# Kernel tuning notes

Measured on AMD Instinct MI355X. Metric: run time of the kernel, lower is better.

## Reference

```python
import jax, jax.numpy as jnp
import numpy as np

B, N = 1, 512
NODE_DIM, EDGE_DIM = 384, 128
H, SK, SV, PK, PV = 8, 16, 16, 4, 4
EPS = 1e-8
LN_EPS = 1e-5


def setup_inputs() -> dict:
    key = jax.random.key(0)
    ks = jax.random.split(key, 20)
    d, e = NODE_DIM, EDGE_DIM
    s = 0.02
    rn = lambda k, sh: jax.random.normal(k, sh, jnp.float32) * s
    # orthonormal per-residue rotations (valid rigid frames)
    R, _ = jnp.linalg.qr(jax.random.normal(ks[2], (B, N, 3, 3), jnp.float32))
    out_dim = H * (SV + EDGE_DIM + PV * 4)  # scalar + pairwise + points(3) + point norms(1)
    return dict(
        node_features=jax.random.normal(ks[0], (B, N, d), jnp.float32),
        edge_features=jax.random.normal(ks[1], (B, N, N, e), jnp.float32),
        rotations=R,
        translations=jax.random.normal(ks[3], (B, N, 3), jnp.float32),
        mask=jnp.ones((B, N), bool),
        Wq_s=rn(ks[4], (d, H * SK)), Wk_s=rn(ks[5], (d, H * SK)), Wv_s=rn(ks[6], (d, H * SV)),
        Wq_p=rn(ks[7], (d, H * PK * 3)), Wk_p=rn(ks[8], (d, H * PK * 3)), Wv_p=rn(ks[9], (d, H * PV * 3)),
        point_weights=jnp.full((H,), np.log(np.e - 1.0), jnp.float32),  # softplus -> 1
        Wb=rn(ks[10], (e, H)), bb=jnp.zeros((H,), jnp.float32),
        Wo=rn(ks[11], (out_dim, d)), bo=jnp.zeros((d,), jnp.float32),
        g1=jnp.ones((d,), jnp.float32), beta1=jnp.zeros((d,), jnp.float32),
        W1=rn(ks[12], (d, 2 * d)), b1=jnp.zeros((2 * d,), jnp.float32),
        W2=rn(ks[13], (2 * d, 2 * d)), b2=jnp.zeros((2 * d,), jnp.float32),
        W3=rn(ks[14], (2 * d, d)), b3=jnp.zeros((d,), jnp.float32),
        g2=jnp.ones((d,), jnp.float32), beta2=jnp.zeros((d,), jnp.float32),
    )


def _layer_norm(x, g, b):
    mu = x.mean(-1, keepdims=True)
    var = ((x - mu) ** 2).mean(-1, keepdims=True)
    return (x - mu) * jax.lax.rsqrt(var + LN_EPS) * g + b


def _forward(node_features, edge_features, rotations, translations, mask,
             Wq_s, Wk_s, Wv_s, Wq_p, Wk_p, Wv_p, point_weights, Wb, bb, Wo, bo,
             g1, beta1, W1, b1, W2, b2, W3, b3, g2, beta2):
    b, n, d = node_features.shape
    # num_attn_logits = 3 (scalar + point + pairwise)
    scal_scale = (3 * SK) ** -0.5
    point_scale = (3 * PK * 4.5) ** -0.5
    pair_scale = 3 ** -0.5

    qs = (node_features @ Wq_s).reshape(b, n, H, SK)
    kk = (node_features @ Wk_s).reshape(b, n, H, SK)
    vs = (node_features @ Wv_s).reshape(b, n, H, SV)

    def apply_rigid(p):  # p: (b,n,h,d,3); global = R^T applied per lucidrains einsum + t
        return jnp.einsum('bnhdc,bncr->bnhdr', p, rotations) + translations[:, :, None, None, :]

    qp = apply_rigid((node_features @ Wq_p).reshape(b, n, H, PK, 3))
    kp = apply_rigid((node_features @ Wk_p).reshape(b, n, H, PK, 3))
    vp = apply_rigid((node_features @ Wv_p).reshape(b, n, H, PV, 3))

    logits = jnp.einsum('bihk,bjhk->bhij', qs, kk) * scal_scale

    # point distance term: sum_{d,c} (q-k)^2 = |q|^2 + |k|^2 - 2 q.k (avoids (b,h,i,j,d,3) tensor)
    w = jax.nn.softplus(point_weights)  # (H,)
    q2 = jnp.einsum('bnhdc,bnhdc->bhn', qp, qp)
    k2 = jnp.einsum('bnhdc,bnhdc->bhn', kp, kp)
    cross = jnp.einsum('bihdc,bjhdc->bhij', qp, kp)
    dist = q2[..., :, None] + k2[..., None, :] - 2.0 * cross  # (b,h,i,j)
    logits = logits - 0.5 * point_scale * w[None, :, None, None] * dist

    pair_bias = (jnp.einsum('bije,eh->bhij', edge_features, Wb) + bb[None, :, None, None]) * pair_scale
    logits = logits + pair_bias

    pm = mask[:, None, :, None] & mask[:, None, None, :]  # (b,1,i,j)
    logits = jnp.where(pm, logits, -jnp.finfo(logits.dtype).max)
    attn = jax.nn.softmax(logits, axis=-1)  # (b,h,i,j)

    rs = jnp.einsum('bhij,bjhv->bihv', attn, vs).reshape(b, n, H * SV)
    rp = jnp.einsum('bhij,bije->bihe', attn, edge_features).reshape(b, n, H * EDGE_DIM)
    pts = jnp.einsum('bhij,bjhdc->bihdc', attn, vp)
    # invert rigid: subtract t, apply R (inverse of R^T application)
    local = jnp.einsum('bihdc,birc->bihdr', pts - translations[:, :, None, None, :], rotations)
    norms = jnp.sqrt((local ** 2).sum(-1) + EPS)  # (b,n,H,PV)

    cat = jnp.concatenate([rs, local.reshape(b, n, H * PV * 3), norms.reshape(b, n, H * PV), rp], axis=-1)
    ipa_out = cat @ Wo + bo

    x = _layer_norm(ipa_out, g1, beta1)  # dropout is identity at eval
    x = jax.nn.relu(x @ W1 + b1)
    x = jax.nn.relu(x @ W2 + b2)
    x = x @ W3 + b3
    return _layer_norm(x, g2, beta2)


def reference(node_features, edge_features, rotations, translations, mask,
              Wq_s, Wk_s, Wv_s, Wq_p, Wk_p, Wv_p, point_weights, Wb, bb, Wo, bo,
              g1, beta1, W1, b1, W2, b2, W3, b3, g2, beta2):
    return _forward(node_features, edge_features, rotations, translations, mask,
                    Wq_s, Wk_s, Wv_s, Wq_p, Wk_p, Wv_p, point_weights, Wb, bb, Wo, bo,
                    g1, beta1, W1, b1, W2, b2, W3, b3, g2, beta2)
```

## Files before the change

kernel.cpp:

```cpp
#include <hip/hip_runtime.h>
#include <cstddef>

#define NN 512
#define DD 384
#define EE 128
#define HH 8

static constexpr float SCAL_SCALE  = 0.1443375673f;
static constexpr float POINT_SCALE = 0.1360827635f;
static constexpr float PAIR_SCALE  = 0.5773502692f;
static constexpr float LN_EPS = 1e-5f;
static constexpr float EPS    = 1e-8f;

typedef __bf16 bf16x8 __attribute__((ext_vector_type(8)));
typedef float  f32x4  __attribute__((ext_vector_type(4)));

__device__ __forceinline__ unsigned short bf16_bits(float v) {
    union { __bf16 b; unsigned short s; } c; c.b = (__bf16)v; return c.s;
}

__global__ __launch_bounds__(256) void prep_weights_kernel(
    const float* __restrict__ Wo, const float* __restrict__ W1,
    const float* __restrict__ W2, const float* __restrict__ W3,
    const float* __restrict__ Wq_s, const float* __restrict__ Wk_s,
    const float* __restrict__ Wv_s,
    const float* __restrict__ Wq_p, const float* __restrict__ Wk_p,
    const float* __restrict__ Wv_p,
    unsigned short* __restrict__ WoT, unsigned short* __restrict__ W1T,
    unsigned short* __restrict__ W2T, unsigned short* __restrict__ W3T,
    unsigned short* __restrict__ WprojT)
{
    const int b = blockIdx.x;
    const float* W; unsigned short* out;
    int K, N, tile, rowoff = 0;
    if (b < 480)       { W = Wo;   out = WoT;    K = 1280; N = 384; tile = b; }
    else if (b < 768)  { W = W1;   out = W1T;    K = 384;  N = 768; tile = b - 480; }
    else if (b < 1344) { W = W2;   out = W2T;    K = 768;  N = 768; tile = b - 768; }
    else if (b < 1632) { W = W3;   out = W3T;    K = 768;  N = 384; tile = b - 1344; }
    else if (b < 1680) { W = Wq_s; out = WprojT; K = 384;  N = 128; tile = b - 1632; rowoff = 0; }
    else if (b < 1728) { W = Wk_s; out = WprojT; K = 384;  N = 128; tile = b - 1680; rowoff = 128; }
    else if (b < 1776) { W = Wv_s; out = WprojT; K = 384;  N = 128; tile = b - 1728; rowoff = 256; }
    else if (b < 1812) { W = Wq_p; out = WprojT; K = 384;  N = 96;  tile = b - 1776; rowoff = 384; }
    else if (b < 1848) { W = Wk_p; out = WprojT; K = 384;  N = 96;  tile = b - 1812; rowoff = 480; }
    else               { W = Wv_p; out = WprojT; K = 384;  N = 96;  tile = b - 1848; rowoff = 576; }

    const int ntn = N / 32;
    const int n0 = (tile % ntn) * 32, k0 = (tile / ntn) * 32;
    __shared__ float tb[32][33];
    const int tx = threadIdx.x & 31, ty = threadIdx.x >> 5;
    #pragma unroll
    for (int dy = 0; dy < 32; dy += 8)
        tb[ty + dy][tx] = W[(size_t)(k0 + ty + dy) * N + n0 + tx];
    __syncthreads();
    #pragma unroll
    for (int dy = 0; dy < 32; dy += 8)
        out[(size_t)(rowoff + n0 + ty + dy) * K + k0 + tx] = bf16_bits(tb[tx][ty + dy]);
}

template <int K, int NOUT, bool RELU, bool HASB>
__global__ __launch_bounds__(256) void gemm_mfma2(
    const float* __restrict__ X, const unsigned short* __restrict__ Wt,
    const float* __restrict__ bias, float* __restrict__ Y)
{
    const int t = threadIdx.x;
    const int w = t >> 6, lane = t & 63;
    const int r = lane & 15, q = lane >> 4;
    const int n0 = blockIdx.x * 16;
    const int m0 = blockIdx.y * 64;

    __shared__ unsigned short Xs[64 * 40];
    __shared__ unsigned short Ws[16 * 40];

    const int row_s = t >> 2, seg_s = t & 3;
    f32x4 acc = {0.f, 0.f, 0.f, 0.f};

    for (int ks = 0; ks < K / 32; ks++) {
        __syncthreads();
        {
            const float* src = X + (size_t)(m0 + row_s) * K + ks * 32 + seg_s * 8;
            float4 a = *(const float4*)src;
            float4 b = *(const float4*)(src + 4);
            union { bf16x8 v; uint4 u; } pk;
            pk.v[0] = (__bf16)a.x; pk.v[1] = (__bf16)a.y;
            pk.v[2] = (__bf16)a.z; pk.v[3] = (__bf16)a.w;
            pk.v[4] = (__bf16)b.x; pk.v[5] = (__bf16)b.y;
            pk.v[6] = (__bf16)b.z; pk.v[7] = (__bf16)b.w;
            *(uint4*)&Xs[row_s * 40 + seg_s * 8] = pk.u;
            if (t < 64)
                *(uint4*)&Ws[row_s * 40 + seg_s * 8] =
                    *(const uint4*)&Wt[(size_t)(n0 + row_s) * K + ks * 32 + seg_s * 8];
        }
        __syncthreads();
        bf16x8 a = *(const bf16x8*)&Xs[(w * 16 + r) * 40 + q * 8];
        bf16x8 b = *(const bf16x8*)&Ws[r * 40 + q * 8];
        acc = __builtin_amdgcn_mfma_f32_16x16x32_bf16(a, b, acc, 0, 0, 0);
    }
    const float bi = HASB ? bias[n0 + r] : 0.f;
    #pragma unroll
    for (int reg = 0; reg < 4; reg++) {
        const int m = m0 + w * 16 + q * 4 + reg;
        float v = acc[reg] + bi;
        if (RELU) v = fmaxf(v, 0.f);
        Y[(size_t)m * NOUT + n0 + r] = v;
    }
}

__global__ __launch_bounds__(256) void ipa_post_kernel(
    const float* __restrict__ proj_out, const float* __restrict__ rot,
    const float* __restrict__ trans, const float* __restrict__ pw,
    const float* __restrict__ bb,
    unsigned short* __restrict__ Qp, unsigned short* __restrict__ Kp,
    unsigned short* __restrict__ svT)
{
    const int i = blockIdx.x;
    const int t = threadIdx.x;
    __shared__ float outs[672];
    __shared__ float ptg[288];
    __shared__ float q2s[8], k2s[8], pwh[8];

    for (int f = t; f < 672; f += 256) outs[f] = proj_out[(size_t)i * 672 + f];
    if (t < 8) pwh[t] = 0.5f * POINT_SCALE * log1pf(expf(pw[t]));
    __syncthreads();

    for (int f = t; f < 288; f += 256) {
        int which = f / 96, idx = f % 96;
        int hd = idx / 3, r = idx % 3;
        float acc = trans[(size_t)i * 3 + r];
        #pragma unroll
        for (int c = 0; c < 3; c++)
            acc += outs[384 + which * 96 + hd * 3 + c] * rot[(size_t)i * 9 + c * 3 + r];
        ptg[f] = acc;
    }
    __syncthreads();
    if (t < 16) {
        int which = t / 8, h = t % 8;
        float acc = 0.f;
        #pragma unroll
        for (int m = 0; m < 12; m++) {
            float v = ptg[which * 96 + h * 12 + m];
            acc += v * v;
        }
        (which ? k2s : q2s)[h] = acc;
    }
    __syncthreads();

    {
        const int h = t >> 5, d = t & 31;
        float qv, kv;
        if (d < 16)      { qv = outs[h * 16 + d] * SCAL_SCALE; kv = outs[128 + h * 16 + d]; }
        else if (d < 28) { qv = ptg[h * 12 + d - 16] * (2.f * pwh[h]); kv = ptg[96 + h * 12 + d - 16]; }
        else if (d == 28){ qv = -pwh[h] * q2s[h]; kv = 1.f; }
        else if (d == 29){ qv = 1.f; kv = -pwh[h] * k2s[h]; }
        else if (d == 30){ qv = 1.f; kv = bb[h] * PAIR_SCALE; }
        else             { qv = 0.f; kv = 0.f; }
        Qp[((size_t)i * 8 + h) * 32 + d] = bf16_bits(qv);
        Kp[((size_t)i * 8 + h) * 32 + d] = bf16_bits(kv);
    }
    if (t < 128) {
        int h = t >> 4, v = t & 15;
        svT[((size_t)h * 32 + v) * NN + i] = bf16_bits(outs[256 + h * 16 + v]);
    } else if (t < 224) {
        int idx = t - 128, h = idx / 12, m = idx % 12;
        svT[((size_t)h * 32 + 16 + m) * NN + i] = bf16_bits(ptg[192 + idx]);
    }
}

__global__ __launch_bounds__(256) void ipa_logits_mfma(
    const float* __restrict__ edge,
    const unsigned short* __restrict__ Qp, const unsigned short* __restrict__ Kp,
    const float* __restrict__ Wb, float* __restrict__ att)
{
    const int t = threadIdx.x;
    const int w = t >> 6;
    const int lane = t & 63;
    const int r = lane & 15, q = lane >> 4;
    const int j0 = blockIdx.x * 32, i0 = blockIdx.y * 16;

    __shared__ unsigned short edA[128 * 128];
    __shared__ unsigned short wbT[16 * 128];
    __shared__ float Lb[8 * 16 * 33];

    for (int idx = t; idx < 2048; idx += 256) {
        int h = idx >> 7, e = idx & 127;
        float v = (h < 8) ? Wb[e * 8 + h] * PAIR_SCALE : 0.f;
        wbT[h * 128 + e] = bf16_bits(v);
    }
    __syncthreads();

    bf16x8 wbf[4];
    #pragma unroll
    for (int s = 0; s < 4; s++)
        wbf[s] = *(const bf16x8*)&wbT[r * 128 + s * 32 + q * 8];

    const int ii = t >> 4, seg = t & 15;
    for (int sub = 0; sub < 4; sub++) {
        __syncthreads();
        #pragma unroll 2
        for (int it = 0; it < 8; it++) {
            const float* src = edge + (((size_t)(i0 + ii) * NN) + (j0 + sub * 8 + it)) * EE + seg * 8;
            float4 x0 = *(const float4*)src;
            float4 x1 = *(const float4*)(src + 4);
            union { bf16x8 v; uint4 u; } pk;
            pk.v[0] = (__bf16)x0.x; pk.v[1] = (__bf16)x0.y;
            pk.v[2] = (__bf16)x0.z; pk.v[3] = (__bf16)x0.w;
            pk.v[4] = (__bf16)x1.x; pk.v[5] = (__bf16)x1.y;
            pk.v[6] = (__bf16)x1.z; pk.v[7] = (__bf16)x1.w;
            int row = it * 16 + ii;
            int cp = seg ^ ii;
            *(uint4*)&edA[row * 128 + cp * 8] = pk.u;
        }
        __syncthreads();
        for (int jj = 0; jj < 2; jj++) {
            const int jloc = w * 2 + jj;
            f32x4 acc = {0.f, 0.f, 0.f, 0.f};
            #pragma unroll
            for (int s = 0; s < 4; s++) {
                bf16x8 a = *(const bf16x8*)&edA[(jloc * 16 + r) * 128 + (((s * 4 + q) ^ r) * 8)];
                acc = __builtin_amdgcn_mfma_f32_16x16x32_bf16(a, wbf[s], acc, 0, 0, 0);
            }
            if (r < 8) {
                #pragma unroll
                for (int reg = 0; reg < 4; reg++)
                    Lb[(r * 16 + q * 4 + reg) * 33 + sub * 8 + jloc] = acc[reg];
            }
        }
    }
    __syncthreads();
    for (int t4 = 0; t4 < 4; t4++) {
        const int idx = w * 4 + t4;
        const int h = idx >> 1, jt = idx & 1;
        bf16x8 aq = *(const bf16x8*)&Qp[((size_t)(i0 + r) * 8 + h) * 32 + q * 8];
        bf16x8 bk = *(const bf16x8*)&Kp[((size_t)(j0 + jt * 16 + r) * 8 + h) * 32 + q * 8];
        f32x4 acc = {0.f, 0.f, 0.f, 0.f};
        acc = __builtin_amdgcn_mfma_f32_16x16x32_bf16(aq, bk, acc, 0, 0, 0);
        #pragma unroll
        for (int reg = 0; reg < 4; reg++)
            Lb[(h * 16 + q * 4 + reg) * 33 + jt * 16 + r] += acc[reg];
    }
    __syncthreads();
    for (int g = t; g < 4096; g += 256) {
        int h = g >> 9, i = (g >> 5) & 15, j = g & 31;
        att[((size_t)h * NN + i0 + i) * NN + j0 + j] = Lb[(h * 16 + i) * 33 + j];
    }
}

__global__ __launch_bounds__(256) void ipa_softmax_kernel(
    const float* __restrict__ att, unsigned short* __restrict__ attn_bf)
{
    __shared__ float red[4];
    __shared__ float bc;
    const size_t row = blockIdx.x;
    const float* p = att + row * NN;
    const int t = threadIdx.x;

    float a = p[t], b = p[t + 256];
    float m = fmaxf(a, b);
    #pragma unroll
    for (int off = 32; off; off >>= 1) m = fmaxf(m, __shfl_down(m, off, 64));
    if ((t & 63) == 0) red[t >> 6] = m;
    __syncthreads();
    if (t == 0) bc = fmaxf(fmaxf(red[0], red[1]), fmaxf(red[2], red[3]));
    __syncthreads();
    m = bc;
    float e0 = expf(a - m), e1 = expf(b - m);
    float s = e0 + e1;
    #pragma unroll
    for (int off = 32; off; off >>= 1) s += __shfl_down(s, off, 64);
    __syncthreads();
    if ((t & 63) == 0) red[t >> 6] = s;
    __syncthreads();
    if (t == 0) bc = red[0] + red[1] + red[2] + red[3];
    __syncthreads();
    const float inv = 1.f / bc;
    attn_bf[row * NN + t]       = bf16_bits(e0 * inv);
    attn_bf[row * NN + t + 256] = bf16_bits(e1 * inv);
}

__global__ __launch_bounds__(256) void ipa_sv_mfma(
    const unsigned short* __restrict__ attn_bf, const unsigned short* __restrict__ svT,
    float* __restrict__ cat, float* __restrict__ pts)
{
    const int t = threadIdx.x;
    const int w = t >> 6, lane = t & 63;
    const int r = lane & 15, q = lane >> 4;
    const int h = blockIdx.y;
    const int mt = w & 1, nt = w >> 1;
    const int i0 = blockIdx.x * 32 + mt * 16;

    f32x4 acc = {0.f, 0.f, 0.f, 0.f};
    for (int ks = 0; ks < 16; ks++) {
        const int k0 = ks * 32 + q * 8;
        bf16x8 a = *(const bf16x8*)&attn_bf[((size_t)h * NN + i0 + r) * NN + k0];
        bf16x8 b = *(const bf16x8*)&svT[((size_t)h * 32 + nt * 16 + r) * NN + k0];
        acc = __builtin_amdgcn_mfma_f32_16x16x32_bf16(a, b, acc, 0, 0, 0);
    }
    if (nt == 0) {
        #pragma unroll
        for (int reg = 0; reg < 4; reg++)
            cat[(size_t)(i0 + q * 4 + reg) * 1280 + h * 16 + r] = acc[reg];
    } else if (r < 12) {
        #pragma unroll
        for (int reg = 0; reg < 4; reg++)
            pts[(size_t)(i0 + q * 4 + reg) * 96 + h * 12 + r] = acc[reg];
    }
}

__global__ __launch_bounds__(256) void ipa_rp_mfma(
    const unsigned short* __restrict__ attn_bf, const float* __restrict__ edge,
    float* __restrict__ cat)
{
    const int i = blockIdx.x;
    const int t = threadIdx.x;
    const int w = t >> 6, lane = t & 63;
    const int r = lane & 15, q = lane >> 4;
    const int nt0 = w * 2;

    __shared__ __bf16 eb[64 * 136];

    f32x4 acc0 = {0.f, 0.f, 0.f, 0.f}, acc1 = {0.f, 0.f, 0.f, 0.f};
    const int jj_s = t >> 2, seg_s = t & 3;

    for (int jb = 0; jb < 8; jb++) {
        __syncthreads();
        {
            const float* src = edge + ((size_t)i * NN + jb * 64 + jj_s) * EE + seg_s * 32;
            #pragma unroll
            for (int u = 0; u < 4; u++) {
                float4 a = ((const float4*)src)[u * 2];
                float4 b = ((const float4*)src)[u * 2 + 1];
                union { bf16x8 v; uint4 uu; } pk;
                pk.v[0] = (__bf16)a.x; pk.v[1] = (__bf16)a.y;
                pk.v[2] = (__bf16)a.z; pk.v[3] = (__bf16)a.w;
                pk.v[4] = (__bf16)b.x; pk.v[5] = (__bf16)b.y;
                pk.v[6] = (__bf16)b.z; pk.v[7] = (__bf16)b.w;
                *(uint4*)&eb[jj_s * 136 + seg_s * 32 + u * 8] = pk.uu;
            }
        }
        __syncthreads();
        #pragma unroll
        for (int kh = 0; kh < 2; kh++) {
            const int k0 = jb * 64 + kh * 32;
            bf16x8 a = *(const bf16x8*)&attn_bf[((size_t)r * NN + i) * NN + k0 + q * 8];
            bf16x8 b0, b1;
            #pragma unroll
            for (int jj = 0; jj < 8; jj++) {
                const int jl = kh * 32 + q * 8 + jj;
                b0[jj] = eb[jl * 136 + nt0 * 16 + r];
                b1[jj] = eb[jl * 136 + (nt0 + 1) * 16 + r];
            }
            acc0 = __builtin_amdgcn_mfma_f32_16x16x32_bf16(a, b0, acc0, 0, 0, 0);
            acc1 = __builtin_amdgcn_mfma_f32_16x16x32_bf16(a, b1, acc1, 0, 0, 0);
        }
    }
    if (q < 2) {
        #pragma unroll
        for (int reg = 0; reg < 4; reg++) {
            const int h = q * 4 + reg;
            cat[(size_t)i * 1280 + 256 + h * 128 + nt0 * 16 + r]       = acc0[reg];
            cat[(size_t)i * 1280 + 256 + h * 128 + (nt0 + 1) * 16 + r] = acc1[reg];
        }
    }
}

__global__ __launch_bounds__(256) void ipa_local_kernel(
    const float* __restrict__ pts, const float* __restrict__ rot,
    const float* __restrict__ trans, float* __restrict__ cat)
{
    const int t = threadIdx.x;
    const int i = blockIdx.x * 2 + (t >> 7);
    const int l = t & 127;
    const float* tr = trans + (size_t)i * 3;
    const float* R  = rot + (size_t)i * 9;
    const float* P  = pts + (size_t)i * 96;
    if (l < 96) {
        int hd = l / 3, rr = l % 3;
        float acc = 0.f;
        #pragma unroll
        for (int c = 0; c < 3; c++)
            acc += (P[hd * 3 + c] - tr[c]) * R[rr * 3 + c];
        cat[(size_t)i * 1280 + 128 + l] = acc;
    } else {
        int pv = l - 96;
        float s = EPS;
        #pragma unroll
        for (int rr = 0; rr < 3; rr++) {
            float v = 0.f;
            #pragma unroll
            for (int c = 0; c < 3; c++)
                v += (P[pv * 3 + c] - tr[c]) * R[rr * 3 + c];
            s += v * v;
        }
        cat[(size_t)i * 1280 + 224 + pv] = sqrtf(s);
    }
}

__global__ __launch_bounds__(256) void ln_kernel(
    const float* __restrict__ X, const float* __restrict__ g,
    const float* __restrict__ beta, float* __restrict__ Y, int Dim)
{
    __shared__ float red[4];
    __shared__ float bc;
    const int i = blockIdx.x;
    const int t = threadIdx.x;
    const float* x = X + (size_t)i * Dim;

    float s = 0.f;
    for (int k = t; k < Dim; k += 256) s += x[k];
    #pragma unroll
    for (int off = 32; off; off >>= 1) s += __shfl_down(s, off, 64);
    if ((t & 63) == 0) red[t >> 6] = s;
    __syncthreads();
    if (t == 0) bc = red[0] + red[1] + red[2] + red[3];
    __syncthreads();
    const float mu = bc / Dim;

    float v = 0.f;
    for (int k = t; k < Dim; k += 256) { float d = x[k] - mu; v += d * d; }
    #pragma unroll
    for (int off = 32; off; off >>= 1) v += __shfl_down(v, off, 64);
    __syncthreads();
    if ((t & 63) == 0) red[t >> 6] = v;
    __syncthreads();
    if (t == 0) bc = red[0] + red[1] + red[2] + red[3];
    __syncthreads();
    const float rstd = rsqrtf(bc / Dim + LN_EPS);

    for (int k = t; k < Dim; k += 256)
        Y[(size_t)i * Dim + k] = (x[k] - mu) * rstd * g[k] + beta[k];
}

extern "C" void kernel_launch(void* const* d_in, const int* in_sizes, int n_in,
                              void* d_out, int out_size, void* d_ws, size_t ws_size,
                              hipStream_t stream)
{
    const float* nf    = (const float*)d_in[0];
    const float* edge  = (const float*)d_in[1];
    const float* rot   = (const float*)d_in[2];
    const float* trans = (const float*)d_in[3];
    const float* Wq_s = (const float*)d_in[5];
    const float* Wk_s = (const float*)d_in[6];
    const float* Wv_s = (const float*)d_in[7];
    const float* Wq_p = (const float*)d_in[8];
    const float* Wk_p = (const float*)d_in[9];
    const float* Wv_p = (const float*)d_in[10];
    const float* pw   = (const float*)d_in[11];
    const float* Wb   = (const float*)d_in[12];
    const float* bb   = (const float*)d_in[13];
    const float* Wo   = (const float*)d_in[14];
    const float* bo   = (const float*)d_in[15];
    const float* g1   = (const float*)d_in[16];
    const float* be1  = (const float*)d_in[17];
    const float* W1   = (const float*)d_in[18];
    const float* b1   = (const float*)d_in[19];
    const float* W2   = (const float*)d_in[20];
    const float* b2   = (const float*)d_in[21];
    const float* W3   = (const float*)d_in[22];
    const float* b3   = (const float*)d_in[23];
    const float* g2   = (const float*)d_in[24];
    const float* be2  = (const float*)d_in[25];

    float* ws = (float*)d_ws;
    float* att      = ws;
    float* pts      = att + 2097152;
    float* cat      = pts + 49152;
    float* ipa      = cat + 655360;
    float* x1       = ipa + 196608;
    float* h1       = x1  + 196608;
    float* h2       = h1  + 393216;
    float* y        = h2  + 393216;
    float* proj_out = y   + 196608;
    unsigned short* attn_bf = (unsigned short*)(proj_out + 344064);
    unsigned short* Qp  = attn_bf + 2097152;
    unsigned short* Kp  = Qp  + 131072;
    unsigned short* svT = Kp  + 131072;
    unsigned short* WoT = svT + 131072;
    unsigned short* W1T = WoT + 491520;
    unsigned short* W2T = W1T + 294912;
    unsigned short* W3T = W2T + 589824;
    unsigned short* WprojT = W3T + 294912;

    prep_weights_kernel<<<1884, 256, 0, stream>>>(Wo, W1, W2, W3,
                                                  Wq_s, Wk_s, Wv_s, Wq_p, Wk_p, Wv_p,
                                                  WoT, W1T, W2T, W3T, WprojT);

    gemm_mfma2<384, 672, false, false><<<dim3(42, 8), 256, 0, stream>>>(nf, WprojT, nullptr, proj_out);

    ipa_post_kernel<<<NN, 256, 0, stream>>>(proj_out, rot, trans, pw, bb, Qp, Kp, svT);

    ipa_logits_mfma<<<dim3(16, 32), 256, 0, stream>>>(edge, Qp, Kp, Wb, att);

    ipa_softmax_kernel<<<HH * NN, 256, 0, stream>>>(att, attn_bf);

    ipa_sv_mfma<<<dim3(16, 8), 256, 0, stream>>>(attn_bf, svT, cat, pts);
    ipa_rp_mfma<<<NN, 256, 0, stream>>>(attn_bf, edge, cat);
    ipa_local_kernel<<<256, 256, 0, stream>>>(pts, rot, trans, cat);

    gemm_mfma2<1280, 384, false, true><<<dim3(24, 8), 256, 0, stream>>>(cat, WoT, bo, ipa);
    ln_kernel<<<NN, 256, 0, stream>>>(ipa, g1, be1, x1, 384);

    gemm_mfma2<384, 768, true, true><<<dim3(48, 8), 256, 0, stream>>>(x1, W1T, b1, h1);
    gemm_mfma2<768, 768, true, true><<<dim3(48, 8), 256, 0, stream>>>(h1, W2T, b2, h2);
    gemm_mfma2<768, 384, false, true><<<dim3(24, 8), 256, 0, stream>>>(h2, W3T, b3, y);

    ln_kernel<<<NN, 256, 0, stream>>>(y, g2, be2, (float*)d_out, 384);
}
```

Measured before the change: 385.1 us.

## Fuse IPA logits, softmax and value aggregation into split-K flash-style kernel

Replaces the separate logits, softmax, scalar/point value, and pairwise aggregation kernels with one fused kernel using online softmax over j-chunks. Edge features are read once and reused for both the bias logits and the pairwise output. Partial outputs from 8 j-splits are then combined by a merge kernel. This removes the full attention matrix round trips and the second edge read. In exchange it does the pairwise aggregation with scalar FMAs instead of MFMA, needs many block-wide syncs per small chunk, and writes a large partial-output buffer.

New measurement: 375.5 us. 1.03x faster.

```diff
diff --git a/kernel.cpp b/kernel.cpp
--- a/kernel.cpp
+++ b/kernel.cpp
@@ -17,6 +17,9 @@
 
 __device__ __forceinline__ unsigned short bf16_bits(float v) {
     union { __bf16 b; unsigned short s; } c; c.b = (__bf16)v; return c.s;
+}
+__device__ __forceinline__ float bits2f(unsigned u) {
+    union { unsigned u; float f; } c; c.u = u; return c.f;
 }
 
 __global__ __launch_bounds__(256) void prep_weights_kernel(
@@ -165,26 +168,32 @@
     }
 }
 
-__global__ __launch_bounds__(256) void ipa_logits_mfma(
+__global__ __launch_bounds__(256) void ipa_fused(
     const float* __restrict__ edge,
     const unsigned short* __restrict__ Qp, const unsigned short* __restrict__ Kp,
-    const float* __restrict__ Wb, float* __restrict__ att)
-{
+    const unsigned short* __restrict__ svT, const float* __restrict__ Wb,
+    float* __restrict__ Opart, float* __restrict__ Mpart, float* __restrict__ Lpart)
+{
+    const int js = blockIdx.x;
+    const int it = blockIdx.y;
+    const int i0 = it * 8;
+    const int jbase = js * 64;
     const int t = threadIdx.x;
-    const int w = t >> 6;
-    const int lane = t & 63;
+    const int w = t >> 6, lane = t & 63;
     const int r = lane & 15, q = lane >> 4;
-    const int j0 = blockIdx.x * 32, i0 = blockIdx.y * 16;
-
-    __shared__ unsigned short edA[128 * 128];
+
+    __shared__ unsigned short edA[8 * 8 * 128];
     __shared__ unsigned short wbT[16 * 128];
-    __shared__ float Lb[8 * 16 * 33];
+    __shared__ unsigned short svj[8 * 28 * 8];
+    __shared__ float Lb[8 * 8 * 9];
+    __shared__ float mrow[64], lrow[64], arow[64];
 
     for (int idx = t; idx < 2048; idx += 256) {
         int h = idx >> 7, e = idx & 127;
         float v = (h < 8) ? Wb[e * 8 + h] * PAIR_SCALE : 0.f;
         wbT[h * 128 + e] = bf16_bits(v);
     }
+    if (t < 64) { mrow[t] = -1e30f; lrow[t] = 0.f; }
     __syncthreads();
 
     bf16x8 wbf[4];
@@ -192,12 +201,37 @@
     for (int s = 0; s < 4; s++)
         wbf[s] = *(const bf16x8*)&wbT[r * 128 + s * 32 + q * 8];
 
-    const int ii = t >> 4, seg = t & 15;
-    for (int sub = 0; sub < 4; sub++) {
-        __syncthreads();
-        #pragma unroll 2
-        for (int it = 0; it < 8; it++) {
-            const float* src = edge + (((size_t)(i0 + ii) * NN) + (j0 + sub * 8 + it)) * EE + seg * 8;
+    bf16x8 aq[2];
+    #pragma unroll
+    for (int hh = 0; hh < 2; hh++)
+        aq[hh] = *(const bf16x8*)&Qp[((size_t)(i0 + (r & 7)) * 8 + (w * 2 + hh)) * 32 + q * 8];
+
+    const int ai = t >> 5, hgrp = (t >> 4) & 1, ec = t & 15;
+    float rp_acc[4][8];
+    #pragma unroll
+    for (int a = 0; a < 4; a++)
+        #pragma unroll
+        for (int e = 0; e < 8; e++) rp_acc[a][e] = 0.f;
+    const int l32 = t & 31;
+    float sv_acc[7];
+    int sh[7], sc[7];
+    #pragma unroll
+    for (int s = 0; s < 7; s++) {
+        int g = l32 * 7 + s;
+        sh[s] = g / 28; sc[s] = g % 28;
+        sv_acc[s] = 0.f;
+    }
+
+    const int sj = t >> 5, sih = (t >> 4) & 1, sseg = t & 15;
+
+    for (int st = 0; st < 8; st++) {
+        const int j0 = jbase + st * 8;
+        __syncthreads();
+
+        #pragma unroll
+        for (int il = 0; il < 4; il++) {
+            const int si = sih * 4 + il;
+            const float* src = edge + (((size_t)(i0 + si) * NN) + (j0 + sj)) * EE + sseg * 8;
             float4 x0 = *(const float4*)src;
             float4 x1 = *(const float4*)(src + 4);
             union { bf16x8 v; uint4 u; } pk;
@@ -205,160 +239,159 @@
             pk.v[2] = (__bf16)x0.z; pk.v[3] = (__bf16)x0.w;
             pk.v[4] = (__bf16)x1.x; pk.v[5] = (__bf16)x1.y;
             pk.v[6] = (__bf16)x1.z; pk.v[7] = (__bf16)x1.w;
-            int row = it * 16 + ii;
-            int cp = seg ^ ii;
+            const int row = sj * 8 + si;
+            const int cp = sseg ^ (row & 15);
             *(uint4*)&edA[row * 128 + cp * 8] = pk.u;
         }
-        __syncthreads();
-        for (int jj = 0; jj < 2; jj++) {
-            const int jloc = w * 2 + jj;
+        if (t < 224) {
+            const int h = t / 28, c = t % 28;
+            *(uint4*)&svj[(h * 28 + c) * 8] =
+                *(const uint4*)&svT[(size_t)(h * 32 + c) * NN + j0];
+        }
+        __syncthreads();
+
+        {
             f32x4 acc = {0.f, 0.f, 0.f, 0.f};
             #pragma unroll
             for (int s = 0; s < 4; s++) {
-                bf16x8 a = *(const bf16x8*)&edA[(jloc * 16 + r) * 128 + (((s * 4 + q) ^ r) * 8)];
+                bf16x8 a = *(const bf16x8*)&edA[(w * 16 + r) * 128 + (((s * 4 + q) ^ r) * 8)];
                 acc = __builtin_amdgcn_mfma_f32_16x16x32_bf16(a, wbf[s], acc, 0, 0, 0);
             }
             if (r < 8) {
                 #pragma unroll
+                for (int reg = 0; reg < 4; reg++) {
+                    const int m = q * 4 + reg;
+                    Lb[(r * 8 + (m & 7)) * 9 + (w * 2 + (m >> 3))] = acc[reg];
+                }
+            }
+        }
+        __syncthreads();
+
+        #pragma unroll
+        for (int hh = 0; hh < 2; hh++) {
+            const int h = w * 2 + hh;
+            bf16x8 bk = *(const bf16x8*)&Kp[((size_t)(j0 + (r & 7)) * 8 + h) * 32 + q * 8];
+            f32x4 acc = {0.f, 0.f, 0.f, 0.f};
+            acc = __builtin_amdgcn_mfma_f32_16x16x32_bf16(aq[hh], bk, acc, 0, 0, 0);
+            if (r < 8 && q < 2) {
+                #pragma unroll
                 for (int reg = 0; reg < 4; reg++)
-                    Lb[(r * 16 + q * 4 + reg) * 33 + sub * 8 + jloc] = acc[reg];
+                    Lb[(h * 8 + q * 4 + reg) * 9 + r] += acc[reg];
             }
         }
-    }
-    __syncthreads();
-    for (int t4 = 0; t4 < 4; t4++) {
-        const int idx = w * 4 + t4;
-        const int h = idx >> 1, jt = idx & 1;
-        bf16x8 aq = *(const bf16x8*)&Qp[((size_t)(i0 + r) * 8 + h) * 32 + q * 8];
-        bf16x8 bk = *(const bf16x8*)&Kp[((size_t)(j0 + jt * 16 + r) * 8 + h) * 32 + q * 8];
-        f32x4 acc = {0.f, 0.f, 0.f, 0.f};
-        acc = __builtin_amdgcn_mfma_f32_16x16x32_bf16(aq, bk, acc, 0, 0, 0);
-        #pragma unroll
-        for (int reg = 0; reg < 4; reg++)
-            Lb[(h * 16 + q * 4 + reg) * 33 + jt * 16 + r] += acc[reg];
-    }
-    __syncthreads();
-    for (int g = t; g < 4096; g += 256) {
-        int h = g >> 9, i = (g >> 5) & 15, j = g & 31;
-        att[((size_t)h * NN + i0 + i) * NN + j0 + j] = Lb[(h * 16 + i) * 33 + j];
-    }
-}
-
-__global__ __launch_bounds__(256) void ipa_softmax_kernel(
-    const float* __restrict__ att, unsigned short* __restrict__ attn_bf)
-{
-    __shared__ float red[4];
-    __shared__ float bc;
-    const size_t row = blockIdx.x;
-    const float* p = att + row * NN;
+        __syncthreads();
+
+        if (t < 64) {
+            float lg[8];
+            #pragma unroll
+            for (int j = 0; j < 8; j++) lg[j] = Lb[t * 9 + j];
+            float mx = lg[0];
+            #pragma unroll
+            for (int j = 1; j < 8; j++) mx = fmaxf(mx, lg[j]);
+            const float mold = mrow[t];
+            const float mnew = fmaxf(mold, mx);
+            const float al = expf(mold - mnew);
+            float sum = 0.f;
+            #pragma unroll
+            for (int j = 0; j < 8; j++) {
+                float p = expf(lg[j] - mnew);
+                Lb[t * 9 + j] = p;
+                sum += p;
+            }
+            lrow[t] = lrow[t] * al + sum;
+            mrow[t] = mnew;
+            arow[t] = al;
+        }
+        __syncthreads();
+
+        #pragma unroll
+        for (int a = 0; a < 4; a++) {
+            const float al = arow[(hgrp * 4 + a) * 8 + ai];
+            #pragma unroll
+            for (int e = 0; e < 8; e++) rp_acc[a][e] *= al;
+        }
+        #pragma unroll
+        for (int s = 0; s < 7; s++) sv_acc[s] *= arow[sh[s] * 8 + ai];
+
+        #pragma unroll
+        for (int j = 0; j < 8; j++) {
+            const int row = j * 8 + ai;
+            uint4 ev = *(const uint4*)&edA[row * 128 + ((ec ^ (row & 15)) * 8)];
+            float ef[8];
+            ef[0] = bits2f(ev.x << 16); ef[1] = bits2f(ev.x & 0xffff0000u);
+            ef[2] = bits2f(ev.y << 16); ef[3] = bits2f(ev.y & 0xffff0000u);
+            ef[4] = bits2f(ev.z << 16); ef[5] = bits2f(ev.z & 0xffff0000u);
+            ef[6] = bits2f(ev.w << 16); ef[7] = bits2f(ev.w & 0xffff0000u);
+            #pragma unroll
+            for (int a = 0; a < 4; a++) {
+                const float p = Lb[((hgrp * 4 + a) * 8 + ai) * 9 + j];
+                #pragma unroll
+                for (int e = 0; e < 8; e++) rp_acc[a][e] += p * ef[e];
+            }
+            #pragma unroll
+            for (int s = 0; s < 7; s++) {
+                const float p = Lb[(sh[s] * 8 + ai) * 9 + j];
+                const float v = bits2f((unsigned)svj[(sh[s] * 28 + sc[s]) * 8 + j] << 16);
+                sv_acc[s] += p * v;
+            }
+        }
+    }
+
+    float* orow = Opart + ((size_t)((js * 64 + it) * 8 + ai)) * 1248;
+    #pragma unroll
+    for (int a = 0; a < 4; a++) {
+        const int h = hgrp * 4 + a;
+        #pragma unroll
+        for (int e = 0; e < 8; e++)
+            orow[h * 156 + 28 + ec * 8 + e] = rp_acc[a][e];
+    }
+    #pragma unroll
+    for (int s = 0; s < 7; s++)
+        orow[sh[s] * 156 + sc[s]] = sv_acc[s];
+    if (t < 64) {
+        Mpart[(size_t)(js * 64 + it) * 64 + t] = mrow[t];
+        Lpart[(size_t)(js * 64 + it) * 64 + t] = lrow[t];
+    }
+}
+
+__global__ __launch_bounds__(256) void ipa_merge(
+    const float* __restrict__ Opart, const float* __restrict__ Mpart,
+    const float* __restrict__ Lpart, float* __restrict__ cat,
+    float* __restrict__ pts)
+{
+    const int i = blockIdx.x;
+    const int itile = i >> 3, il = i & 7;
     const int t = threadIdx.x;
-
-    float a = p[t], b = p[t + 256];
-    float m = fmaxf(a, b);
-    #pragma unroll
-    for (int off = 32; off; off >>= 1) m = fmaxf(m, __shfl_down(m, off, 64));
-    if ((t & 63) == 0) red[t >> 6] = m;
-    __syncthreads();
-    if (t == 0) bc = fmaxf(fmaxf(red[0], red[1]), fmaxf(red[2], red[3]));
-    __syncthreads();
-    m = bc;
-    float e0 = expf(a - m), e1 = expf(b - m);
-    float s = e0 + e1;
-    #pragma unroll
-    for (int off = 32; off; off >>= 1) s += __shfl_down(s, off, 64);
-    __syncthreads();
-    if ((t & 63) == 0) red[t >> 6] = s;
-    __syncthreads();
-    if (t == 0) bc = red[0] + red[1] + red[2] + red[3];
-    __syncthreads();
-    const float inv = 1.f / bc;
-    attn_bf[row * NN + t]       = bf16_bits(e0 * inv);
-    attn_bf[row * NN + t + 256] = bf16_bits(e1 * inv);
-}
-
-__global__ __launch_bounds__(256) void ipa_sv_mfma(
-    const unsigned short* __restrict__ attn_bf, const unsigned short* __restrict__ svT,
-    float* __restrict__ cat, float* __restrict__ pts)
-{
-    const int t = threadIdx.x;
-    const int w = t >> 6, lane = t & 63;
-    const int r = lane & 15, q = lane >> 4;
-    const int h = blockIdx.y;
-    const int mt = w & 1, nt = w >> 1;
-    const int i0 = blockIdx.x * 32 + mt * 16;
-
-    f32x4 acc = {0.f, 0.f, 0.f, 0.f};
-    for (int ks = 0; ks < 16; ks++) {
-        const int k0 = ks * 32 + q * 8;
-        bf16x8 a = *(const bf16x8*)&attn_bf[((size_t)h * NN + i0 + r) * NN + k0];
-        bf16x8 b = *(const bf16x8*)&svT[((size_t)h * 32 + nt * 16 + r) * NN + k0];
-        acc = __builtin_amdgcn_mfma_f32_16x16x32_bf16(a, b, acc, 0, 0, 0);
-    }
-    if (nt == 0) {
-        #pragma unroll
-        for (int reg = 0; reg < 4; reg++)
-            cat[(size_t)(i0 + q * 4 + reg) * 1280 + h * 16 + r] = acc[reg];
-    } else if (r < 12) {
-        #pragma unroll
-        for (int reg = 0; reg < 4; reg++)
-            pts[(size_t)(i0 + q * 4 + reg) * 96 + h * 12 + r] = acc[reg];
-    }
-}
-
-__global__ __launch_bounds__(256) void ipa_rp_mfma(
-    const unsigned short* __restrict__ attn_bf, const float* __restrict__ edge,
-    float* __restrict__ cat)
-{
-    const int i = blockIdx.x;
-    const int t = threadIdx.x;
-    const int w = t >> 6, lane = t & 63;
-    const int r = lane & 15, q = lane >> 4;
-    const int nt0 = w * 2;
-
-    __shared__ __bf16 eb[64 * 136];
-
-    f32x4 acc0 = {0.f, 0.f, 0.f, 0.f}, acc1 = {0.f, 0.f, 0.f, 0.f};
-    const int jj_s = t >> 2, seg_s = t & 3;
-
-    for (int jb = 0; jb < 8; jb++) {
-        __syncthreads();
-        {
-            const float* src = edge + ((size_t)i * NN + jb * 64 + jj_s) * EE + seg_s * 32;
-            #pragma unroll
-            for (int u = 0; u < 4; u++) {
-                float4 a = ((const float4*)src)[u * 2];
-                float4 b = ((const float4*)src)[u * 2 + 1];
-                union { bf16x8 v; uint4 uu; } pk;
-                pk.v[0] = (__bf16)a.x; pk.v[1] = (__bf16)a.y;
-                pk.v[2] = (__bf16)a.z; pk.v[3] = (__bf16)a.w;
-                pk.v[4] = (__bf16)b.x; pk.v[5] = (__bf16)b.y;
-                pk.v[6] = (__bf16)b.z; pk.v[7] = (__bf16)b.w;
-                *(uint4*)&eb[jj_s * 136 + seg_s * 32 + u * 8] = pk.uu;
-            }
-        }
-        __syncthreads();
-        #pragma unroll
-        for (int kh = 0; kh < 2; kh++) {
-            const int k0 = jb * 64 + kh * 32;
-            bf16x8 a = *(const bf16x8*)&attn_bf[((size_t)r * NN + i) * NN + k0 + q * 8];
-            bf16x8 b0, b1;
-            #pragma unroll
-            for (int jj = 0; jj < 8; jj++) {
-                const int jl = kh * 32 + q * 8 + jj;
-                b0[jj] = eb[jl * 136 + nt0 * 16 + r];
-                b1[jj] = eb[jl * 136 + (nt0 + 1) * 16 + r];
-            }
-            acc0 = __builtin_amdgcn_mfma_f32_16x16x32_bf16(a, b0, acc0, 0, 0, 0);
-            acc1 = __builtin_amdgcn_mfma_f32_16x16x32_bf16(a, b1, acc1, 0, 0, 0);
-        }
-    }
-    if (q < 2) {
-        #pragma unroll
-        for (int reg = 0; reg < 4; reg++) {
-            const int h = q * 4 + reg;
-            cat[(size_t)i * 1280 + 256 + h * 128 + nt0 * 16 + r]       = acc0[reg];
-            cat[(size_t)i * 1280 + 256 + h * 128 + (nt0 + 1) * 16 + r] = acc1[reg];
-        }
+    __shared__ float wn[64];
+
+    if (t < 8) {
+        const int h = t;
+        float ms[8], ls[8], M = -1e30f;
+        #pragma unroll
+        for (int s = 0; s < 8; s++) {
+            ms[s] = Mpart[(size_t)(s * 64 + itile) * 64 + h * 8 + il];
+            ls[s] = Lpart[(size_t)(s * 64 + itile) * 64 + h * 8 + il];
+            M = fmaxf(M, ms[s]);
+        }
+        float denom = 0.f, e[8];
+        #pragma unroll
+        for (int s = 0; s < 8; s++) { e[s] = expf(ms[s] - M); denom += e[s] * ls[s]; }
+        const float inv = 1.f / denom;
+        #pragma unroll
+        for (int s = 0; s < 8; s++) wn[h * 8 + s] = e[s] * inv;
+    }
+    __syncthreads();
+
+    for (int col = t; col < 1248; col += 256) {
+        const int h = col / 156, c = col % 156;
+        float acc = 0.f;
+        #pragma unroll
+        for (int s = 0; s < 8; s++)
+            acc += wn[h * 8 + s] *
+                   Opart[((size_t)(s * 64 + itile) * 8 + il) * 1248 + col];
+        if (c < 16)      cat[(size_t)i * 1280 + h * 16 + c] = acc;
+        else if (c < 28) pts[(size_t)i * 96 + h * 12 + (c - 16)] = acc;
+        else             cat[(size_t)i * 1280 + 256 + h * 128 + (c - 28)] = acc;
     }
 }
 
@@ -460,17 +493,18 @@
     const float* be2  = (const float*)d_in[25];
 
     float* ws = (float*)d_ws;
-    float* att      = ws;
-    float* pts      = att + 2097152;
-    float* cat      = pts + 49152;
-    float* ipa      = cat + 655360;
+    float* cat      = ws;
+    float* pts      = cat + 655360;
+    float* ipa      = pts + 49152;
     float* x1       = ipa + 196608;
     float* h1       = x1  + 196608;
     float* h2       = h1  + 393216;
     float* y        = h2  + 393216;
     float* proj_out = y   + 196608;
-    unsigned short* attn_bf = (unsigned short*)(proj_out + 344064);
-    unsigned short* Qp  = attn_bf + 2097152;
+    float* Opart    = proj_out + 344064;
+    float* Mpart    = Opart + 5111808;
+    float* Lpart    = Mpart + 32768;
+    unsigned short* Qp  = (unsigned short*)(Lpart + 32768);
     unsigned short* Kp  = Qp  + 131072;
     unsigned short* svT = Kp  + 131072;
     unsigned short* WoT = svT + 131072;
@@ -487,12 +521,10 @@
 
     ipa_post_kernel<<<NN, 256, 0, stream>>>(proj_out, rot, trans, pw, bb, Qp, Kp, svT);
 
-    ipa_logits_mfma<<<dim3(16, 32), 256, 0, stream>>>(edge, Qp, Kp, Wb, att);
-
-    ipa_softmax_kernel<<<HH * NN, 256, 0, stream>>>(att, attn_bf);
-
-    ipa_sv_mfma<<<dim3(16, 8), 256, 0, stream>>>(attn_bf, svT, cat, pts);
-    ipa_rp_mfma<<<NN, 256, 0, stream>>>(attn_bf, edge, cat);
+    ipa_fused<<<dim3(8, 64), 256, 0, stream>>>(edge, Qp, Kp, svT, Wb,
+                                               Opart, Mpart, Lpart);
+
+    ipa_merge<<<NN, 256, 0, stream>>>(Opart, Mpart, Lpart, cat, pts);
     ipa_local_kernel<<<256, 256, 0, stream>>>(pts, rot, trans, cat);
 
     gemm_mfma2<1280, 384, false, true><<<dim3(24, 8), 256, 0, stream>>>(cat, WoT, bo, ipa);
```
